# Optimization experiments

Measured on AMD Instinct MI355X. Metric: run time of the kernel, lower is better.

## Reference

```python
import jax, jax.numpy as jnp
import numpy as np

EPS = 1e-8

def setup_inputs() -> dict:
    key = jax.random.key(0)
    k1, k2, k3, k4, k5 = jax.random.split(key, 5)
    B, S, d, H = 4, 1024, 512, 8
    hd = d // H
    x = jax.random.normal(k1, (B, S, d), dtype=jnp.float32)
    V = jax.random.normal(k2, (B, S, H, hd), dtype=jnp.float32)
    # binary biological mask [B, S, S]
    M = (jax.random.uniform(k3, (B, S, S)) > 0.5).astype(jnp.float32)
    in_proj_w = jax.random.normal(k4, (3 * d, d), dtype=jnp.float32) * 0.02
    in_proj_b = jnp.zeros((3 * d,), dtype=jnp.float32)
    out_w = jax.random.normal(k5, (d, d), dtype=jnp.float32) * 0.02
    out_b = jnp.zeros((d,), dtype=jnp.float32)
    return {"x": x, "V": V, "M": M, "in_proj_w": in_proj_w,
            "in_proj_b": in_proj_b, "out_w": out_w, "out_b": out_b}


def reference(x, V, M, in_proj_w, in_proj_b, out_w, out_b):
    B, S, d = x.shape
    H, hd = V.shape[2], V.shape[3]
    # packed QKV projection (torch MHA in_proj); V slice is computed by torch
    # but its result is discarded, so only Q,K slices influence the output.
    qkv = x @ in_proj_w.T + in_proj_b            # [B, S, 3d]
    q = qkv[..., :d].reshape(B, S, H, hd).transpose(0, 2, 1, 3)        # [B,H,S,hd]
    k = qkv[..., d:2 * d].reshape(B, S, H, hd).transpose(0, 2, 1, 3)   # [B,H,S,hd]
    scores = jnp.einsum("bhqd,bhkd->bhqk", q, k) / jnp.sqrt(jnp.float32(hd))
    A = jax.nn.softmax(scores, axis=-1)           # [B,H,S,S] per-head attn weights
    # biological mask + L1 renormalization (post-hoc, as in original)
    A_sparse = A * M[:, None, :, :]
    norm = jnp.sum(jnp.abs(A_sparse), axis=-1, keepdims=True) + EPS
    A_bar = A_sparse / norm
    # custom V: [B,S,H,hd] -> [B,H,S,hd]
    Vp = V.transpose(0, 2, 1, 3)
    out = jnp.einsum("bhqk,bhkd->bhqd", A_bar, Vp)  # [B,H,S,hd]
    out = out.transpose(0, 2, 1, 3).reshape(B, S, d)
    return out @ out_w.T + out_b
```

## Files before the change

kernel.cpp:

```cpp
#include <hip/hip_runtime.h>
#include <hip/hip_bf16.h>

#define BB 4
#define SS 1024
#define DD 512
#define HH 8
#define HD 64

typedef __attribute__((ext_vector_type(8))) short bf16x8;
typedef __attribute__((ext_vector_type(4))) float f32x4;

static __device__ __forceinline__ unsigned short f2b(float f) {
  union { float f; unsigned int u; } c; c.f = f;
  return (unsigned short)((c.u + 0x7fffu + ((c.u >> 16) & 1u)) >> 16);
}

__global__ __launch_bounds__(256) void prep(
    const float* __restrict__ x, const float* __restrict__ W1,
    const float* __restrict__ Wo, const float* __restrict__ Mmask,
    const float* __restrict__ V, unsigned short* __restrict__ xb,
    unsigned short* __restrict__ W1b, unsigned short* __restrict__ Wob,
    unsigned char* __restrict__ Mpack, unsigned short* __restrict__ Vt) {
  __shared__ float Ls[64][65];
  const int bid = blockIdx.x;
  const int tid = threadIdx.x;

  if (bid < 1408) {
    const float* src; unsigned short* dst; size_t off;
    if (bid < 1024) { src = x;  dst = xb;  off = ((size_t)bid * 256 + tid) * 8; }
    else if (bid < 1280) { src = W1; dst = W1b; off = ((size_t)(bid - 1024) * 256 + tid) * 8; }
    else { src = Wo; dst = Wob; off = ((size_t)(bid - 1280) * 256 + tid) * 8; }
    const float4 a = *(const float4*)(src + off);
    const float4 b = *(const float4*)(src + off + 4);
    union { unsigned short s[8]; uint4 v; } o;
    o.s[0] = f2b(a.x); o.s[1] = f2b(a.y); o.s[2] = f2b(a.z); o.s[3] = f2b(a.w);
    o.s[4] = f2b(b.x); o.s[5] = f2b(b.y); o.s[6] = f2b(b.z); o.s[7] = f2b(b.w);
    *(uint4*)(dst + off) = o.v;
  } else if (bid < 3456) {
    const size_t g = (size_t)(bid - 1408) * 256 + tid;
    const float4 a = *(const float4*)(Mmask + g * 8);
    const float4 b = *(const float4*)(Mmask + g * 8 + 4);
    unsigned v = 0;
    v |= (a.x > 0.5f) ? 1u : 0u;   v |= (a.y > 0.5f) ? 2u : 0u;
    v |= (a.z > 0.5f) ? 4u : 0u;   v |= (a.w > 0.5f) ? 8u : 0u;
    v |= (b.x > 0.5f) ? 16u : 0u;  v |= (b.y > 0.5f) ? 32u : 0u;
    v |= (b.z > 0.5f) ? 64u : 0u;  v |= (b.w > 0.5f) ? 128u : 0u;
    Mpack[g] = (unsigned char)v;
  } else {
    const int id = bid - 3456;
    const int s0 = (id & 15) * 64, h = (id >> 4) & 7, b = id >> 7;
    {
      const int r = tid >> 2, cs = (tid & 3) * 16;
      const float* src = V + ((size_t)((b * SS + s0 + r) * HH) + h) * HD + cs;
#pragma unroll
      for (int j = 0; j < 4; j++) {
        const float4 v = *(const float4*)(src + j * 4);
        Ls[r][cs + j * 4 + 0] = v.x; Ls[r][cs + j * 4 + 1] = v.y;
        Ls[r][cs + j * 4 + 2] = v.z; Ls[r][cs + j * 4 + 3] = v.w;
      }
    }
    __syncthreads();
    {
      const int d = tid >> 2, ss = (tid & 3) * 16;
      union { unsigned short s[16]; uint4 v[2]; } o;
#pragma unroll
      for (int j = 0; j < 16; j++) o.s[j] = f2b(Ls[ss + j][d]);
      unsigned short* dst =
          Vt + ((size_t)((b * HH + h) * HD + d)) * SS + s0 + ss;
      *(uint4*)dst = o.v[0];
      *(uint4*)(dst + 8) = o.v[1];
    }
  }
}

__global__ __launch_bounds__(256) void gemm_qk(
    const unsigned short* __restrict__ xb, const unsigned short* __restrict__ W1b,
    const float* __restrict__ bias, unsigned short* __restrict__ qkb) {
  __shared__ unsigned short As[128][40];
  __shared__ unsigned short Bs[64][40];
  const int tid = threadIdx.x;
  const int lane = tid & 63, wave = tid >> 6;
  const int l16 = lane & 15, quad = lane >> 4;
  const int row0 = blockIdx.y * 128, col0 = blockIdx.x * 64;

  f32x4 acc[2][4];
#pragma unroll
  for (int i = 0; i < 2; i++)
#pragma unroll
    for (int j = 0; j < 4; j++) acc[i][j] = (f32x4){0.f, 0.f, 0.f, 0.f};

  const int ra = tid >> 1, csa = (tid & 1) * 16;
  const int rb = tid >> 2, csb = (tid & 3) * 8;
  const unsigned short* ap = xb + (size_t)(row0 + ra) * DD + csa;
  const unsigned short* bp = W1b + (size_t)(col0 + rb) * DD + csb;

  uint4 pa0 = *(const uint4*)ap, pa1 = *(const uint4*)(ap + 8);
  uint4 pb = *(const uint4*)bp;

  for (int k0 = 0; k0 < DD; k0 += 32) {
    __syncthreads();
    *(uint4*)&As[ra][csa] = pa0;
    *(uint4*)&As[ra][csa + 8] = pa1;
    *(uint4*)&Bs[rb][csb] = pb;
    __syncthreads();
    if (k0 + 32 < DD) {
      pa0 = *(const uint4*)(ap + k0 + 32);
      pa1 = *(const uint4*)(ap + k0 + 40);
      pb = *(const uint4*)(bp + k0 + 32);
    }

    const bf16x8 a0 = *(const bf16x8*)&As[wave * 32 + l16][quad * 8];
    const bf16x8 a1 = *(const bf16x8*)&As[wave * 32 + 16 + l16][quad * 8];
#pragma unroll
    for (int nt = 0; nt < 4; nt++) {
      const bf16x8 bb = *(const bf16x8*)&Bs[nt * 16 + l16][quad * 8];
      acc[0][nt] = __builtin_amdgcn_mfma_f32_16x16x32_bf16(a0, bb, acc[0][nt], 0, 0, 0);
      acc[1][nt] = __builtin_amdgcn_mfma_f32_16x16x32_bf16(a1, bb, acc[1][nt], 0, 0, 0);
    }
  }

#pragma unroll
  for (int nt = 0; nt < 4; nt++) {
    const int col = col0 + nt * 16 + l16;
    const float bv = bias[col];
    const float scale = (col < DD) ? 0.125f : 1.0f;
#pragma unroll
    for (int mi = 0; mi < 2; mi++)
#pragma unroll
      for (int reg = 0; reg < 4; reg++) {
        const int row = row0 + wave * 32 + mi * 16 + quad * 4 + reg;
        qkb[(size_t)row * 1024 + col] = f2b((acc[mi][nt][reg] + bv) * scale);
      }
  }
}

__global__ __launch_bounds__(256) void gemm_out(
    const unsigned short* __restrict__ Ab, const unsigned short* __restrict__ Wob,
    const float* __restrict__ bias, float* __restrict__ out) {
  __shared__ unsigned short As[64][40];
  __shared__ unsigned short Bs[64][40];
  const int tid = threadIdx.x;
  const int lane = tid & 63, wave = tid >> 6;
  const int l16 = lane & 15, quad = lane >> 4;
  const int row0 = blockIdx.y * 64, col0 = blockIdx.x * 64;

  f32x4 acc[4];
#pragma unroll
  for (int j = 0; j < 4; j++) acc[j] = (f32x4){0.f, 0.f, 0.f, 0.f};

  const int r = tid >> 2, cs = (tid & 3) * 8;
  const unsigned short* ap = Ab + (size_t)(row0 + r) * DD + cs;
  const unsigned short* bp = Wob + (size_t)(col0 + r) * DD + cs;

  uint4 pa = *(const uint4*)ap;
  uint4 pb = *(const uint4*)bp;

  for (int k0 = 0; k0 < DD; k0 += 32) {
    __syncthreads();
    *(uint4*)&As[r][cs] = pa;
    *(uint4*)&Bs[r][cs] = pb;
    __syncthreads();
    if (k0 + 32 < DD) {
      pa = *(const uint4*)(ap + k0 + 32);
      pb = *(const uint4*)(bp + k0 + 32);
    }

    const bf16x8 a0 = *(const bf16x8*)&As[wave * 16 + l16][quad * 8];
#pragma unroll
    for (int nt = 0; nt < 4; nt++) {
      const bf16x8 bb = *(const bf16x8*)&Bs[nt * 16 + l16][quad * 8];
      acc[nt] = __builtin_amdgcn_mfma_f32_16x16x32_bf16(a0, bb, acc[nt], 0, 0, 0);
    }
  }

#pragma unroll
  for (int nt = 0; nt < 4; nt++) {
    const int col = col0 + nt * 16 + l16;
    const float bv = bias[col];
#pragma unroll
    for (int reg = 0; reg < 4; reg++) {
      const int row = row0 + wave * 16 + quad * 4 + reg;
      out[(size_t)row * DD + col] = acc[nt][reg] + bv;
    }
  }
}

__global__ __launch_bounds__(512, 4) void flash_attn_fused(
    const unsigned short* __restrict__ qkb, const unsigned short* __restrict__ Vt,
    const unsigned char* __restrict__ Mpack, unsigned short* __restrict__ attnb) {
  __shared__ unsigned short QP[64][72];
  __shared__ unsigned short P2[64][72];
  __shared__ unsigned short Ks[2][64][72];
  __shared__ unsigned short Vs[2][64][72];
  __shared__ float SmS[2][64];

  const int tid = threadIdx.x;
  const int lane = tid & 63, wave = tid >> 6;
  const int l16 = lane & 15, quad = lane >> 4;
  const int wq = wave & 3, sp = wave >> 2;
  const int q0 = blockIdx.x * 64;
  const int h = blockIdx.y;
  const int b = blockIdx.z;

  const int r2 = tid >> 3, cs2 = (tid & 7) * 8;

  {
    const unsigned short* s = qkb + (size_t)(b * SS + q0 + r2) * 1024 + h * HD + cs2;
    *(uint4*)&QP[r2][cs2] = *(const uint4*)s;
  }

  const unsigned char* mp =
      Mpack + (size_t)(b * SS + q0 + wq * 16 + l16) * 128 + sp * 64;
  uint2 pm = *(const uint2*)mp;

  __syncthreads();
  const bf16x8 bQ0 = *(const bf16x8*)&QP[wq * 16 + l16][quad * 8];
  const bf16x8 bQ1 = *(const bf16x8*)&QP[wq * 16 + l16][32 + quad * 8];
  unsigned short(*Ps)[72] =
      (unsigned short(*)[72])(sp ? &P2[wq * 16][0] : &QP[wq * 16][0]);

  float Smp = 0.f;
  f32x4 O[4];
#pragma unroll
  for (int i = 0; i < 4; i++) O[i] = (f32x4){0.f, 0.f, 0.f, 0.f};

  const unsigned short* kp0 =
      qkb + (size_t)(b * SS + r2) * 1024 + DD + h * HD + cs2;
  const unsigned short* kp1 = kp0 + (size_t)512 * 1024;
  const unsigned short* vp0 =
      Vt + ((size_t)((b * HH + h) * HD + r2)) * SS + cs2;
  const unsigned short* vp1 = vp0 + 512;

  uint4 pk0 = *(const uint4*)kp0, pk1 = *(const uint4*)kp1;
  uint4 pv0 = *(const uint4*)vp0, pv1 = *(const uint4*)vp1;

#pragma unroll
  for (int i = 0; i < 8; i++) {
    __syncthreads();
    *(uint4*)&Ks[0][r2][cs2] = pk0;
    *(uint4*)&Ks[1][r2][cs2] = pk1;
    *(uint4*)&Vs[0][r2][cs2] = pv0;
    *(uint4*)&Vs[1][r2][cs2] = pv1;
    __syncthreads();

    const uint2 pm_cur = pm;
    if (i < 7) {
      pk0 = *(const uint4*)(kp0 + (size_t)(i + 1) * 64 * 1024);
      pk1 = *(const uint4*)(kp1 + (size_t)(i + 1) * 64 * 1024);
      pv0 = *(const uint4*)(vp0 + (i + 1) * 64);
      pv1 = *(const uint4*)(vp1 + (i + 1) * 64);
      pm = *(const uint2*)(mp + (i + 1) * 8);
    }

#pragma unroll
    for (int t = 0; t < 4; t++) {
      const bf16x8 aK0 = *(const bf16x8*)&Ks[sp][t * 16 + l16][quad * 8];
      const bf16x8 aK1 = *(const bf16x8*)&Ks[sp][t * 16 + l16][32 + quad * 8];
      f32x4 a = (f32x4){0.f, 0.f, 0.f, 0.f};
      a = __builtin_amdgcn_mfma_f32_16x16x32_bf16(aK0, bQ0, a, 0, 0, 0);
      a = __builtin_amdgcn_mfma_f32_16x16x32_bf16(aK1, bQ1, a, 0, 0, 0);
      const unsigned nib =
          ((t < 2 ? pm_cur.x : pm_cur.y) >> ((t & 1) * 16 + quad * 4)) & 0xFu;
      float e0 = __expf(a[0]); e0 = (nib & 1u) ? e0 : 0.f;
      float e1 = __expf(a[1]); e1 = (nib & 2u) ? e1 : 0.f;
      float e2 = __expf(a[2]); e2 = (nib & 4u) ? e2 : 0.f;
      float e3 = __expf(a[3]); e3 = (nib & 8u) ? e3 : 0.f;
      Smp += (e0 + e1) + (e2 + e3);
      uint2 w;
      w.x = (unsigned)f2b(e0) | ((unsigned)f2b(e1) << 16);
      w.y = (unsigned)f2b(e2) | ((unsigned)f2b(e3) << 16);
      *(uint2*)&Ps[l16][t * 16 + quad * 4] = w;
    }

    const bf16x8 aP0 = *(const bf16x8*)&Ps[l16][quad * 8];
    const bf16x8 aP1 = *(const bf16x8*)&Ps[l16][32 + quad * 8];
#pragma unroll
    for (int dt = 0; dt < 4; dt++) {
      const bf16x8 bV0 = *(const bf16x8*)&Vs[sp][dt * 16 + l16][quad * 8];
      const bf16x8 bV1 = *(const bf16x8*)&Vs[sp][dt * 16 + l16][32 + quad * 8];
      O[dt] = __builtin_amdgcn_mfma_f32_16x16x32_bf16(aP0, bV0, O[dt], 0, 0, 0);
      O[dt] = __builtin_amdgcn_mfma_f32_16x16x32_bf16(aP1, bV1, O[dt], 0, 0, 0);
    }
  }

  Smp += __shfl_xor(Smp, 16);
  Smp += __shfl_xor(Smp, 32);
  if (lane < 16) SmS[sp][wq * 16 + lane] = Smp;

  __syncthreads();
  float* Of = reinterpret_cast<float*>(&Ks[0][0][0]);
  if (sp == 1) {
#pragma unroll
    for (int dt = 0; dt < 4; dt++)
#pragma unroll
      for (int reg = 0; reg < 4; reg++)
        Of[(wq * 16 + quad * 4 + reg) * 64 + dt * 16 + l16] = O[dt][reg];
  }
  __syncthreads();

  if (sp == 0) {
    float inv[4];
#pragma unroll
    for (int reg = 0; reg < 4; reg++) {
      const int ql = wq * 16 + quad * 4 + reg;
      inv[reg] = 1.0f / (SmS[0][ql] + SmS[1][ql] + 1e-12f);
    }
#pragma unroll
    for (int dt = 0; dt < 4; dt++)
#pragma unroll
      for (int reg = 0; reg < 4; reg++) {
        const int ql = wq * 16 + quad * 4 + reg;
        const float v = (O[dt][reg] + Of[ql * 64 + dt * 16 + l16]) * inv[reg];
        attnb[(size_t)(b * SS + q0 + ql) * DD + h * HD + dt * 16 + l16] = f2b(v);
      }
  }
}

extern "C" void kernel_launch(void* const* d_in, const int* in_sizes, int n_in,
                              void* d_out, int out_size, void* d_ws,
                              size_t ws_size, hipStream_t stream) {
  const float* x = (const float*)d_in[0];
  const float* V = (const float*)d_in[1];
  const float* Mmask = (const float*)d_in[2];
  const float* in_proj_w = (const float*)d_in[3];
  const float* in_proj_b = (const float*)d_in[4];
  const float* out_w = (const float*)d_in[5];
  const float* out_b = (const float*)d_in[6];
  float* out = (float*)d_out;

  unsigned char* ws = (unsigned char*)d_ws;
  unsigned short* qkb   = (unsigned short*)(ws);
  unsigned short* xb    = (unsigned short*)(ws + (8ull << 20));
  unsigned short* W1b   = (unsigned short*)(ws + (12ull << 20));
  unsigned short* Wob   = (unsigned short*)(ws + (13ull << 20));
  unsigned short* Vt    = (unsigned short*)(ws + (14ull << 20));
  unsigned short* attnb = (unsigned short*)(ws + (18ull << 20));
  unsigned char*  Mpack = ws + (38ull << 20) + (256u << 10);

  prep<<<3968, 256, 0, stream>>>(x, in_proj_w, out_w, Mmask, V,
                                 xb, W1b, Wob, Mpack, Vt);
  gemm_qk<<<dim3(16, 32), 256, 0, stream>>>(xb, W1b, in_proj_b, qkb);
  flash_attn_fused<<<dim3(SS / 64, HH, BB), 512, 0, stream>>>(
      qkb, Vt, Mpack, attnb);
  gemm_out<<<dim3(8, 64), 256, 0, stream>>>(attnb, Wob, out_b, out);
}
```

Measured before the change: 135.5 us.

## Load K and V MFMA operands directly from global memory, dropping LDS staging

The attention kernel no longer stages K and V tiles through shared memory with register prefetch and two block barriers per iteration. Each wave now reads its MFMA operands for Q, K, V and the mask straight from global memory, which removes the barriers and shrinks LDS use to the P buffer. The cost is that the four query waves in a block each fetch the same K/V data, so global/L2 traffic per block goes up roughly fourfold. Loads are also no longer software-prefetched a tile ahead, which exposes more memory latency. The Of scratch area now reuses PB, which is sized 2x64x72 shorts (18 KB) while 64x64 floats need 16 KB, so it fits.

Measured after the change: 173.0 us. +27.7%, slower.

```diff
diff --git a/kernel.cpp b/kernel.cpp
--- a/kernel.cpp
+++ b/kernel.cpp
@@ -188,10 +188,7 @@
 __global__ __launch_bounds__(512, 4) void flash_attn_fused(
     const unsigned short* __restrict__ qkb, const unsigned short* __restrict__ Vt,
     const unsigned char* __restrict__ Mpack, unsigned short* __restrict__ attnb) {
-  __shared__ unsigned short QP[64][72];
-  __shared__ unsigned short P2[64][72];
-  __shared__ unsigned short Ks[2][64][72];
-  __shared__ unsigned short Vs[2][64][72];
+  __shared__ unsigned short PB[2][64][72];
   __shared__ float SmS[2][64];
 
   const int tid = threadIdx.x;
@@ -202,65 +199,40 @@
   const int h = blockIdx.y;
   const int b = blockIdx.z;
 
-  const int r2 = tid >> 3, cs2 = (tid & 7) * 8;
-
-  {
-    const unsigned short* s = qkb + (size_t)(b * SS + q0 + r2) * 1024 + h * HD + cs2;
-    *(uint4*)&QP[r2][cs2] = *(const uint4*)s;
-  }
+  const unsigned short* qp =
+      qkb + (size_t)(b * SS + q0 + wq * 16 + l16) * 1024 + h * HD + quad * 8;
+  const bf16x8 bQ0 = *(const bf16x8*)qp;
+  const bf16x8 bQ1 = *(const bf16x8*)(qp + 32);
 
   const unsigned char* mp =
       Mpack + (size_t)(b * SS + q0 + wq * 16 + l16) * 128 + sp * 64;
-  uint2 pm = *(const uint2*)mp;
-
-  __syncthreads();
-  const bf16x8 bQ0 = *(const bf16x8*)&QP[wq * 16 + l16][quad * 8];
-  const bf16x8 bQ1 = *(const bf16x8*)&QP[wq * 16 + l16][32 + quad * 8];
-  unsigned short(*Ps)[72] =
-      (unsigned short(*)[72])(sp ? &P2[wq * 16][0] : &QP[wq * 16][0]);
+
+  const unsigned short* kb =
+      qkb + (size_t)(b * SS + sp * 512 + l16) * 1024 + DD + h * HD + quad * 8;
+  const unsigned short* vb =
+      Vt + ((size_t)((b * HH + h) * HD + l16)) * SS + sp * 512 + quad * 8;
+
+  unsigned short(*Ps)[72] = (unsigned short(*)[72]) & PB[sp][wq * 16][0];
 
   float Smp = 0.f;
   f32x4 O[4];
 #pragma unroll
   for (int i = 0; i < 4; i++) O[i] = (f32x4){0.f, 0.f, 0.f, 0.f};
 
-  const unsigned short* kp0 =
-      qkb + (size_t)(b * SS + r2) * 1024 + DD + h * HD + cs2;
-  const unsigned short* kp1 = kp0 + (size_t)512 * 1024;
-  const unsigned short* vp0 =
-      Vt + ((size_t)((b * HH + h) * HD + r2)) * SS + cs2;
-  const unsigned short* vp1 = vp0 + 512;
-
-  uint4 pk0 = *(const uint4*)kp0, pk1 = *(const uint4*)kp1;
-  uint4 pv0 = *(const uint4*)vp0, pv1 = *(const uint4*)vp1;
-
-#pragma unroll
+#pragma unroll 2
   for (int i = 0; i < 8; i++) {
-    __syncthreads();
-    *(uint4*)&Ks[0][r2][cs2] = pk0;
-    *(uint4*)&Ks[1][r2][cs2] = pk1;
-    *(uint4*)&Vs[0][r2][cs2] = pv0;
-    *(uint4*)&Vs[1][r2][cs2] = pv1;
-    __syncthreads();
-
-    const uint2 pm_cur = pm;
-    if (i < 7) {
-      pk0 = *(const uint4*)(kp0 + (size_t)(i + 1) * 64 * 1024);
-      pk1 = *(const uint4*)(kp1 + (size_t)(i + 1) * 64 * 1024);
-      pv0 = *(const uint4*)(vp0 + (i + 1) * 64);
-      pv1 = *(const uint4*)(vp1 + (i + 1) * 64);
-      pm = *(const uint2*)(mp + (i + 1) * 8);
-    }
+    const uint2 pm = *(const uint2*)(mp + i * 8);
 
 #pragma unroll
     for (int t = 0; t < 4; t++) {
-      const bf16x8 aK0 = *(const bf16x8*)&Ks[sp][t * 16 + l16][quad * 8];
-      const bf16x8 aK1 = *(const bf16x8*)&Ks[sp][t * 16 + l16][32 + quad * 8];
+      const unsigned short* kt = kb + (size_t)(i * 64 + t * 16) * 1024;
+      const bf16x8 aK0 = *(const bf16x8*)kt;
+      const bf16x8 aK1 = *(const bf16x8*)(kt + 32);
       f32x4 a = (f32x4){0.f, 0.f, 0.f, 0.f};
       a = __builtin_amdgcn_mfma_f32_16x16x32_bf16(aK0, bQ0, a, 0, 0, 0);
       a = __builtin_amdgcn_mfma_f32_16x16x32_bf16(aK1, bQ1, a, 0, 0, 0);
       const unsigned nib =
-          ((t < 2 ? pm_cur.x : pm_cur.y) >> ((t & 1) * 16 + quad * 4)) & 0xFu;
+          ((t < 2 ? pm.x : pm.y) >> ((t & 1) * 16 + quad * 4)) & 0xFu;
       float e0 = __expf(a[0]); e0 = (nib & 1u) ? e0 : 0.f;
       float e1 = __expf(a[1]); e1 = (nib & 2u) ? e1 : 0.f;
       float e2 = __expf(a[2]); e2 = (nib & 4u) ? e2 : 0.f;
@@ -276,8 +248,9 @@
     const bf16x8 aP1 = *(const bf16x8*)&Ps[l16][32 + quad * 8];
 #pragma unroll
     for (int dt = 0; dt < 4; dt++) {
-      const bf16x8 bV0 = *(const bf16x8*)&Vs[sp][dt * 16 + l16][quad * 8];
-      const bf16x8 bV1 = *(const bf16x8*)&Vs[sp][dt * 16 + l16][32 + quad * 8];
+      const unsigned short* vt = vb + (size_t)(dt * 16) * 1024 + i * 64;
+      const bf16x8 bV0 = *(const bf16x8*)vt;
+      const bf16x8 bV1 = *(const bf16x8*)(vt + 32);
       O[dt] = __builtin_amdgcn_mfma_f32_16x16x32_bf16(aP0, bV0, O[dt], 0, 0, 0);
       O[dt] = __builtin_amdgcn_mfma_f32_16x16x32_bf16(aP1, bV1, O[dt], 0, 0, 0);
     }
@@ -288,7 +261,7 @@
   if (lane < 16) SmS[sp][wq * 16 + lane] = Smp;
 
   __syncthreads();
-  float* Of = reinterpret_cast<float*>(&Ks[0][0][0]);
+  float* Of = reinterpret_cast<float*>(&PB[0][0][0]);
   if (sp == 1) {
 #pragma unroll
     for (int dt = 0; dt < 4; dt++)
```

## Halve attention block to 256 threads with two query tiles per wave

Applied to the files above, without the earlier changes.

The fused attention kernel now runs 4 waves per block instead of 8, and each wave handles 32 query rows (two 16-row tiles) instead of 16. Each K and V fragment read from shared memory then feeds twice as many MFMAs, and Q is loaded straight from global memory into registers instead of being staged through LDS. This cuts LDS traffic per unit of compute and the per-block wave count, at the cost of more registers per wave, more global loads per thread for staging K/V, and a dropped unroll on the outer loop.

Result: slower. 138.8 us (+2.4%).

```diff
diff --git a/kernel.cpp b/kernel.cpp
--- a/kernel.cpp
+++ b/kernel.cpp
@@ -185,71 +185,83 @@
   }
 }
 
-__global__ __launch_bounds__(512, 4) void flash_attn_fused(
+__global__ __launch_bounds__(256) void flash_attn_fused(
     const unsigned short* __restrict__ qkb, const unsigned short* __restrict__ Vt,
     const unsigned char* __restrict__ Mpack, unsigned short* __restrict__ attnb) {
-  __shared__ unsigned short QP[64][72];
-  __shared__ unsigned short P2[64][72];
   __shared__ unsigned short Ks[2][64][72];
   __shared__ unsigned short Vs[2][64][72];
+  __shared__ unsigned short Pbuf[128][72];
   __shared__ float SmS[2][64];
 
   const int tid = threadIdx.x;
   const int lane = tid & 63, wave = tid >> 6;
   const int l16 = lane & 15, quad = lane >> 4;
-  const int wq = wave & 3, sp = wave >> 2;
+  const int wg = wave & 1, sp = wave >> 1;
   const int q0 = blockIdx.x * 64;
   const int h = blockIdx.y;
   const int b = blockIdx.z;
 
-  const int r2 = tid >> 3, cs2 = (tid & 7) * 8;
-
-  {
-    const unsigned short* s = qkb + (size_t)(b * SS + q0 + r2) * 1024 + h * HD + cs2;
-    *(uint4*)&QP[r2][cs2] = *(const uint4*)s;
-  }
-
-  const unsigned char* mp =
-      Mpack + (size_t)(b * SS + q0 + wq * 16 + l16) * 128 + sp * 64;
-  uint2 pm = *(const uint2*)mp;
-
-  __syncthreads();
-  const bf16x8 bQ0 = *(const bf16x8*)&QP[wq * 16 + l16][quad * 8];
-  const bf16x8 bQ1 = *(const bf16x8*)&QP[wq * 16 + l16][32 + quad * 8];
-  unsigned short(*Ps)[72] =
-      (unsigned short(*)[72])(sp ? &P2[wq * 16][0] : &QP[wq * 16][0]);
-
-  float Smp = 0.f;
-  f32x4 O[4];
-#pragma unroll
-  for (int i = 0; i < 4; i++) O[i] = (f32x4){0.f, 0.f, 0.f, 0.f};
-
+  const unsigned short* qp =
+      qkb + (size_t)(b * SS + q0 + wg * 32 + l16) * 1024 + h * HD + quad * 8;
+  const bf16x8 bQa0 = *(const bf16x8*)qp;
+  const bf16x8 bQa1 = *(const bf16x8*)(qp + 32);
+  const bf16x8 bQb0 = *(const bf16x8*)(qp + 16 * 1024);
+  const bf16x8 bQb1 = *(const bf16x8*)(qp + 16 * 1024 + 32);
+
+  const unsigned char* mpa =
+      Mpack + (size_t)(b * SS + q0 + wg * 32 + l16) * 128 + sp * 64;
+  const unsigned char* mpb = mpa + 16 * 128;
+  uint2 pma = *(const uint2*)mpa;
+  uint2 pmb = *(const uint2*)mpb;
+
+  const int r = tid >> 2, cs = (tid & 3) * 16;
   const unsigned short* kp0 =
-      qkb + (size_t)(b * SS + r2) * 1024 + DD + h * HD + cs2;
+      qkb + (size_t)(b * SS + r) * 1024 + DD + h * HD + cs;
   const unsigned short* kp1 = kp0 + (size_t)512 * 1024;
   const unsigned short* vp0 =
-      Vt + ((size_t)((b * HH + h) * HD + r2)) * SS + cs2;
+      Vt + ((size_t)((b * HH + h) * HD + r)) * SS + cs;
   const unsigned short* vp1 = vp0 + 512;
 
-  uint4 pk0 = *(const uint4*)kp0, pk1 = *(const uint4*)kp1;
-  uint4 pv0 = *(const uint4*)vp0, pv1 = *(const uint4*)vp1;
-
-#pragma unroll
+  uint4 pk0a = *(const uint4*)kp0, pk0b = *(const uint4*)(kp0 + 8);
+  uint4 pk1a = *(const uint4*)kp1, pk1b = *(const uint4*)(kp1 + 8);
+  uint4 pv0a = *(const uint4*)vp0, pv0b = *(const uint4*)(vp0 + 8);
+  uint4 pv1a = *(const uint4*)vp1, pv1b = *(const uint4*)(vp1 + 8);
+
+  unsigned short(*Ps)[72] = (unsigned short(*)[72]) & Pbuf[wave * 32][0];
+
+  float Sma = 0.f, Smb = 0.f;
+  f32x4 Oa[4], Ob[4];
+#pragma unroll
+  for (int i = 0; i < 4; i++) {
+    Oa[i] = (f32x4){0.f, 0.f, 0.f, 0.f};
+    Ob[i] = (f32x4){0.f, 0.f, 0.f, 0.f};
+  }
+
   for (int i = 0; i < 8; i++) {
     __syncthreads();
-    *(uint4*)&Ks[0][r2][cs2] = pk0;
-    *(uint4*)&Ks[1][r2][cs2] = pk1;
-    *(uint4*)&Vs[0][r2][cs2] = pv0;
-    *(uint4*)&Vs[1][r2][cs2] = pv1;
-    __syncthreads();
-
-    const uint2 pm_cur = pm;
+    *(uint4*)&Ks[0][r][cs] = pk0a;
+    *(uint4*)&Ks[0][r][cs + 8] = pk0b;
+    *(uint4*)&Ks[1][r][cs] = pk1a;
+    *(uint4*)&Ks[1][r][cs + 8] = pk1b;
+    *(uint4*)&Vs[0][r][cs] = pv0a;
+    *(uint4*)&Vs[0][r][cs + 8] = pv0b;
+    *(uint4*)&Vs[1][r][cs] = pv1a;
+    *(uint4*)&Vs[1][r][cs + 8] = pv1b;
+    __syncthreads();
+
+    const uint2 ma = pma, mb = pmb;
     if (i < 7) {
-      pk0 = *(const uint4*)(kp0 + (size_t)(i + 1) * 64 * 1024);
-      pk1 = *(const uint4*)(kp1 + (size_t)(i + 1) * 64 * 1024);
-      pv0 = *(const uint4*)(vp0 + (i + 1) * 64);
-      pv1 = *(const uint4*)(vp1 + (i + 1) * 64);
-      pm = *(const uint2*)(mp + (i + 1) * 8);
+      const size_t ko = (size_t)(i + 1) * 64 * 1024;
+      pk0a = *(const uint4*)(kp0 + ko);
+      pk0b = *(const uint4*)(kp0 + ko + 8);
+      pk1a = *(const uint4*)(kp1 + ko);
+      pk1b = *(const uint4*)(kp1 + ko + 8);
+      pv0a = *(const uint4*)(vp0 + (i + 1) * 64);
+      pv0b = *(const uint4*)(vp0 + (i + 1) * 64 + 8);
+      pv1a = *(const uint4*)(vp1 + (i + 1) * 64);
+      pv1b = *(const uint4*)(vp1 + (i + 1) * 64 + 8);
+      pma = *(const uint2*)(mpa + (i + 1) * 8);
+      pmb = *(const uint2*)(mpb + (i + 1) * 8);
     }
 
 #pragma unroll
@@ -257,61 +269,86 @@
       const bf16x8 aK0 = *(const bf16x8*)&Ks[sp][t * 16 + l16][quad * 8];
       const bf16x8 aK1 = *(const bf16x8*)&Ks[sp][t * 16 + l16][32 + quad * 8];
       f32x4 a = (f32x4){0.f, 0.f, 0.f, 0.f};
-      a = __builtin_amdgcn_mfma_f32_16x16x32_bf16(aK0, bQ0, a, 0, 0, 0);
-      a = __builtin_amdgcn_mfma_f32_16x16x32_bf16(aK1, bQ1, a, 0, 0, 0);
-      const unsigned nib =
-          ((t < 2 ? pm_cur.x : pm_cur.y) >> ((t & 1) * 16 + quad * 4)) & 0xFu;
-      float e0 = __expf(a[0]); e0 = (nib & 1u) ? e0 : 0.f;
-      float e1 = __expf(a[1]); e1 = (nib & 2u) ? e1 : 0.f;
-      float e2 = __expf(a[2]); e2 = (nib & 4u) ? e2 : 0.f;
-      float e3 = __expf(a[3]); e3 = (nib & 8u) ? e3 : 0.f;
-      Smp += (e0 + e1) + (e2 + e3);
-      uint2 w;
-      w.x = (unsigned)f2b(e0) | ((unsigned)f2b(e1) << 16);
-      w.y = (unsigned)f2b(e2) | ((unsigned)f2b(e3) << 16);
-      *(uint2*)&Ps[l16][t * 16 + quad * 4] = w;
-    }
-
-    const bf16x8 aP0 = *(const bf16x8*)&Ps[l16][quad * 8];
-    const bf16x8 aP1 = *(const bf16x8*)&Ps[l16][32 + quad * 8];
+      a = __builtin_amdgcn_mfma_f32_16x16x32_bf16(aK0, bQa0, a, 0, 0, 0);
+      a = __builtin_amdgcn_mfma_f32_16x16x32_bf16(aK1, bQa1, a, 0, 0, 0);
+      f32x4 c = (f32x4){0.f, 0.f, 0.f, 0.f};
+      c = __builtin_amdgcn_mfma_f32_16x16x32_bf16(aK0, bQb0, c, 0, 0, 0);
+      c = __builtin_amdgcn_mfma_f32_16x16x32_bf16(aK1, bQb1, c, 0, 0, 0);
+
+      const unsigned sh = (t & 1) * 16 + quad * 4;
+      const unsigned niba = ((t < 2 ? ma.x : ma.y) >> sh) & 0xFu;
+      const unsigned nibb = ((t < 2 ? mb.x : mb.y) >> sh) & 0xFu;
+      float e0 = __expf(a[0]); e0 = (niba & 1u) ? e0 : 0.f;
+      float e1 = __expf(a[1]); e1 = (niba & 2u) ? e1 : 0.f;
+      float e2 = __expf(a[2]); e2 = (niba & 4u) ? e2 : 0.f;
+      float e3 = __expf(a[3]); e3 = (niba & 8u) ? e3 : 0.f;
+      Sma += (e0 + e1) + (e2 + e3);
+      uint2 wa;
+      wa.x = (unsigned)f2b(e0) | ((unsigned)f2b(e1) << 16);
+      wa.y = (unsigned)f2b(e2) | ((unsigned)f2b(e3) << 16);
+      *(uint2*)&Ps[l16][t * 16 + quad * 4] = wa;
+
+      float g0 = __expf(c[0]); g0 = (nibb & 1u) ? g0 : 0.f;
+      float g1 = __expf(c[1]); g1 = (nibb & 2u) ? g1 : 0.f;
+      float g2 = __expf(c[2]); g2 = (nibb & 4u) ? g2 : 0.f;
+      float g3 = __expf(c[3]); g3 = (nibb & 8u) ? g3 : 0.f;
+      Smb += (g0 + g1) + (g2 + g3);
+      uint2 wb;
+      wb.x = (unsigned)f2b(g0) | ((unsigned)f2b(g1) << 16);
+      wb.y = (unsigned)f2b(g2) | ((unsigned)f2b(g3) << 16);
+      *(uint2*)&Ps[16 + l16][t * 16 + quad * 4] = wb;
+    }
+
+    const bf16x8 aPa0 = *(const bf16x8*)&Ps[l16][quad * 8];
+    const bf16x8 aPa1 = *(const bf16x8*)&Ps[l16][32 + quad * 8];
+    const bf16x8 aPb0 = *(const bf16x8*)&Ps[16 + l16][quad * 8];
+    const bf16x8 aPb1 = *(const bf16x8*)&Ps[16 + l16][32 + quad * 8];
 #pragma unroll
     for (int dt = 0; dt < 4; dt++) {
       const bf16x8 bV0 = *(const bf16x8*)&Vs[sp][dt * 16 + l16][quad * 8];
       const bf16x8 bV1 = *(const bf16x8*)&Vs[sp][dt * 16 + l16][32 + quad * 8];
-      O[dt] = __builtin_amdgcn_mfma_f32_16x16x32_bf16(aP0, bV0, O[dt], 0, 0, 0);
-      O[dt] = __builtin_amdgcn_mfma_f32_16x16x32_bf16(aP1, bV1, O[dt], 0, 0, 0);
-    }
-  }
-
-  Smp += __shfl_xor(Smp, 16);
-  Smp += __shfl_xor(Smp, 32);
-  if (lane < 16) SmS[sp][wq * 16 + lane] = Smp;
+      Oa[dt] = __builtin_amdgcn_mfma_f32_16x16x32_bf16(aPa0, bV0, Oa[dt], 0, 0, 0);
+      Oa[dt] = __builtin_amdgcn_mfma_f32_16x16x32_bf16(aPa1, bV1, Oa[dt], 0, 0, 0);
+      Ob[dt] = __builtin_amdgcn_mfma_f32_16x16x32_bf16(aPb0, bV0, Ob[dt], 0, 0, 0);
+      Ob[dt] = __builtin_amdgcn_mfma_f32_16x16x32_bf16(aPb1, bV1, Ob[dt], 0, 0, 0);
+    }
+  }
+
+  Sma += __shfl_xor(Sma, 16);
+  Sma += __shfl_xor(Sma, 32);
+  Smb += __shfl_xor(Smb, 16);
+  Smb += __shfl_xor(Smb, 32);
+  if (lane < 16) {
+    SmS[sp][wg * 32 + lane] = Sma;
+    SmS[sp][wg * 32 + 16 + lane] = Smb;
+  }
 
   __syncthreads();
-  float* Of = reinterpret_cast<float*>(&Ks[0][0][0]);
+  float* Of = reinterpret_cast<float*>(&Pbuf[0][0]);
   if (sp == 1) {
 #pragma unroll
     for (int dt = 0; dt < 4; dt++)
 #pragma unroll
-      for (int reg = 0; reg < 4; reg++)
-        Of[(wq * 16 + quad * 4 + reg) * 64 + dt * 16 + l16] = O[dt][reg];
+      for (int reg = 0; reg < 4; reg++) {
+        const int qa = wg * 32 + quad * 4 + reg;
+        Of[qa * 64 + dt * 16 + l16] = Oa[dt][reg];
+        Of[(qa + 16) * 64 + dt * 16 + l16] = Ob[dt][reg];
+      }
   }
   __syncthreads();
 
   if (sp == 0) {
-    float inv[4];
-#pragma unroll
-    for (int reg = 0; reg < 4; reg++) {
-      const int ql = wq * 16 + quad * 4 + reg;
-      inv[reg] = 1.0f / (SmS[0][ql] + SmS[1][ql] + 1e-12f);
-    }
 #pragma unroll
     for (int dt = 0; dt < 4; dt++)
 #pragma unroll
       for (int reg = 0; reg < 4; reg++) {
-        const int ql = wq * 16 + quad * 4 + reg;
-        const float v = (O[dt][reg] + Of[ql * 64 + dt * 16 + l16]) * inv[reg];
-        attnb[(size_t)(b * SS + q0 + ql) * DD + h * HD + dt * 16 + l16] = f2b(v);
+        const int qa = wg * 32 + quad * 4 + reg;
+        const float inva = 1.0f / (SmS[0][qa] + SmS[1][qa] + 1e-12f);
+        const float invb = 1.0f / (SmS[0][qa + 16] + SmS[1][qa + 16] + 1e-12f);
+        const float va = (Oa[dt][reg] + Of[qa * 64 + dt * 16 + l16]) * inva;
+        const float vb = (Ob[dt][reg] + Of[(qa + 16) * 64 + dt * 16 + l16]) * invb;
+        attnb[(size_t)(b * SS + q0 + qa) * DD + h * HD + dt * 16 + l16] = f2b(va);
+        attnb[(size_t)(b * SS + q0 + qa + 16) * DD + h * HD + dt * 16 + l16] = f2b(vb);
       }
   }
 }
@@ -340,7 +377,7 @@
   prep<<<3968, 256, 0, stream>>>(x, in_proj_w, out_w, Mmask, V,
                                  xb, W1b, Wob, Mpack, Vt);
   gemm_qk<<<dim3(16, 32), 256, 0, stream>>>(xb, W1b, in_proj_b, qkb);
-  flash_attn_fused<<<dim3(SS / 64, HH, BB), 512, 0, stream>>>(
+  flash_attn_fused<<<dim3(SS / 64, HH, BB), 256, 0, stream>>>(
       qkb, Vt, Mpack, attnb);
   gemm_out<<<dim3(8, 64), 256, 0, stream>>>(attnb, Wob, out_b, out);
 }
```
